# Kernel tuning notes

Measured on AMD Instinct MI355X. Metric: run time of the kernel, lower is better.

Reference implementation:

```python
import jax, jax.numpy as jnp
import numpy as np

N_NODES = 50000


def gcn_conv(x, W, b, src, dst, n_nodes):
    """PyG GCNConv: h = x @ W; symmetric-normalized aggregation with self-loops; + bias."""
    h = x @ W  # [N, F_out]
    ones = jnp.ones(src.shape[0], dtype=h.dtype)
    # degree including the self-loop (edge weight 1)
    deg = jax.ops.segment_sum(ones, dst, num_segments=n_nodes) + 1.0
    dinv = jax.lax.rsqrt(deg)  # deg >= 1, always valid
    norm = dinv[src] * dinv[dst]  # [E]
    msgs = h[src] * norm[:, None]  # [E, F_out]
    agg = jax.ops.segment_sum(msgs, dst, num_segments=n_nodes)
    agg = agg + h * (dinv * dinv)[:, None]  # self-loop contribution, norm = dinv_i^2
    return agg + b


def setup_inputs() -> dict:
    key = jax.random.key(0)
    ks = jax.random.split(key, 8)
    n, f_in, f_hid, f_out, n_edges = N_NODES, 128, 128, 40, 800000
    x = jax.random.normal(ks[0], (n, f_in), dtype=jnp.float32)
    edge_index = jax.random.randint(ks[1], (2, n_edges), 0, n, dtype=jnp.int64)
    new_edge_indexs = jax.random.randint(ks[2], (2, 1000), 0, n, dtype=jnp.int64)
    # Glorot init like PyG defaults
    s1 = (6.0 / (f_in + f_hid)) ** 0.5
    s2 = (6.0 / (f_hid + f_out)) ** 0.5
    W1 = jax.random.uniform(ks[3], (f_in, f_hid), jnp.float32, -s1, s1)
    b1 = jnp.zeros((f_hid,), jnp.float32)
    W2 = jax.random.uniform(ks[4], (f_hid, f_out), jnp.float32, -s2, s2)
    b2 = jnp.zeros((f_out,), jnp.float32)
    return {"x": x, "W1": W1, "b1": b1, "W2": W2, "b2": b2,
            "edge_index": edge_index, "new_edge_indexs": new_edge_indexs}


def reference(x, W1, b1, W2, b2, edge_index, new_edge_indexs):
    src, dst = edge_index[0], edge_index[1]
    h = gcn_conv(x, W1, b1, src, dst, N_NODES)
    h = jax.nn.relu(h)
    # dropout(p=0.5) is identity in eval mode (training=False)
    h = gcn_conv(h, W2, b2, src, dst, N_NODES)
    return jax.nn.log_softmax(h, axis=-1)
```

## Files before the change

kernel.cpp:

```cpp
#include <hip/hip_runtime.h>
#include <hip/hip_bf16.h>

#define N_NODES 50000
#define N_EDGES 800000
#define F_IN    128
#define F_HID   128
#define F_OUT   40
#define F_OUT_P 64
#define N_TILES (N_NODES / 16)

#define NBIN      98
#define BIN_SHIFT 9
#define EPB       1024
#define CAP       32
#define GBIN_CAP  9216

#define CVT_BLOCKS ((F_IN * F_HID + F_OUT_P * F_HID) / 256)
#define BIN_BLOCKS ((N_EDGES + EPB - 1) / EPB)
#define G1_BLOCKS  ((N_TILES + 3) / 4)

typedef __attribute__((ext_vector_type(8))) short bf16x8;
typedef __attribute__((ext_vector_type(4))) float f32x4;

__device__ __forceinline__ float2 unpack_bf2(unsigned u) {
    float2 r;
    r.x = __uint_as_float(u << 16);
    r.y = __uint_as_float(u & 0xffff0000u);
    return r;
}
__device__ __forceinline__ unsigned pack_bf2(float x, float y) {
    union { unsigned u; __hip_bfloat16 h[2]; } cv;
    cv.h[0] = __float2bfloat16(x);
    cv.h[1] = __float2bfloat16(y);
    return cv.u;
}
__device__ __forceinline__ short bfraw(float v) {
    __hip_bfloat16 h = __float2bfloat16(v);
    return *(short*)&h;
}
__device__ __forceinline__ float bf16u_to_f32(unsigned short us) {
    return __uint_as_float(((unsigned)us) << 16);
}
__device__ __forceinline__ unsigned f32_to_h16(float v) {
    _Float16 h = (_Float16)v;
    return (unsigned)*(unsigned short*)&h;
}
__device__ __forceinline__ float h16_to_f32(unsigned bits) {
    unsigned short us = (unsigned short)bits;
    _Float16 h = *(_Float16*)&us;
    return (float)h;
}

__device__ __forceinline__ int ld_src(const unsigned int* w, int is64, int e) {
    return is64 ? (int)w[2 * e] : (int)w[e];
}
__device__ __forceinline__ int ld_dst(const unsigned int* w, int is64, int e) {
    return is64 ? (int)w[2 * (N_EDGES + e)] : (int)w[N_EDGES + e];
}

__global__ void k_init(const unsigned int* __restrict__ ew,
                       const float* __restrict__ W1, const float* __restrict__ W2,
                       __hip_bfloat16* __restrict__ w1t, __hip_bfloat16* __restrict__ w2t,
                       int* __restrict__ flag, int* __restrict__ gcnt) {
    int b = blockIdx.x, t = threadIdx.x;
    if (b < CVT_BLOCKS) {
        int idx = b * 256 + t;
        if (idx < F_IN * F_HID) {
            int n = idx >> 7, k = idx & 127;
            w1t[idx] = __float2bfloat16(W1[k * F_HID + n]);
        } else {
            int j = idx - F_IN * F_HID;
            int n = j >> 7, k = j & 127;
            w2t[j] = __float2bfloat16(n < F_OUT ? W2[k * F_OUT + n] : 0.f);
        }
        return;
    }
    __shared__ int nz;
    if (t == 0) nz = 0;
    __syncthreads();
    int local = 0;
    for (int i = t; i < 4096; i += 256)
        if (ew[2 * i + 1] != 0u) local = 1;
    if (local) atomicOr(&nz, 1);
    if (t < NBIN) gcnt[t] = 0;
    __syncthreads();
    if (t == 0) flag[0] = (nz == 0) ? 1 : 0;
}

__global__ void k_bing1(const unsigned int* __restrict__ ew, const int* __restrict__ flag,
                        int* __restrict__ gcnt, unsigned* __restrict__ gbin,
                        const float* __restrict__ x, const __hip_bfloat16* __restrict__ w1t,
                        __hip_bfloat16* __restrict__ h1b) {
    __shared__ unsigned buf[NBIN][CAP];
    __shared__ int cnt[NBIN];
    __shared__ int base[NBIN];
    int t = threadIdx.x;
    if (blockIdx.x < BIN_BLOCKS) {
        for (int i = t; i < NBIN; i += 256) cnt[i] = 0;
        __syncthreads();
        int is64 = flag[0];
        int e0 = blockIdx.x * EPB;
        int n = min(EPB, N_EDGES - e0);
        if (n == EPB) {
            int s[4], d[4];
#pragma unroll
            for (int j = 0; j < 4; j++) {
                int e = e0 + t + j * 256;
                s[j] = ld_src(ew, is64, e);
                d[j] = ld_dst(ew, is64, e);
            }
#pragma unroll
            for (int j = 0; j < 4; j++) {
                unsigned rec = (unsigned)s[j] | ((unsigned)d[j] << 16);
                int b = d[j] >> BIN_SHIFT;
                int c = atomicAdd(&cnt[b], 1);
                if (c < CAP) buf[b][c] = rec;
                else {
                    int g = atomicAdd(&gcnt[b], 1);
                    gbin[(size_t)b * GBIN_CAP + g] = rec;
                }
            }
        } else {
            for (int i = t; i < n; i += 256) {
                int e = e0 + i;
                int s = ld_src(ew, is64, e), d = ld_dst(ew, is64, e);
                unsigned rec = (unsigned)s | ((unsigned)d << 16);
                int b = d >> BIN_SHIFT;
                int c = atomicAdd(&cnt[b], 1);
                if (c < CAP) buf[b][c] = rec;
                else {
                    int g = atomicAdd(&gcnt[b], 1);
                    gbin[(size_t)b * GBIN_CAP + g] = rec;
                }
            }
        }
        __syncthreads();
        if (t < NBIN) {
            int m = min(cnt[t], CAP);
            base[t] = atomicAdd(&gcnt[t], m);
            cnt[t] = m;
        }
        __syncthreads();
        int wave = t >> 6, lane = t & 63;
        for (int b = wave; b < NBIN; b += 4) {
            int m = cnt[b], bs = base[b];
            for (int i = lane; i < m; i += 64)
                gbin[(size_t)b * GBIN_CAP + bs + i] = buf[b][i];
        }
        return;
    }
    int wave = t >> 6, lane = t & 63;
    int tile = (blockIdx.x - BIN_BLOCKS) * 4 + wave;
    if (tile >= N_TILES) return;
    int node0 = tile * 16;
    int m = lane & 15, q = lane >> 4;
    bf16x8 A[4];
    const float* arow = x + (size_t)(node0 + m) * F_IN + q * 8;
#pragma unroll
    for (int kt = 0; kt < 4; kt++) {
        float4 f0 = *(const float4*)(arow + kt * 32);
        float4 f1 = *(const float4*)(arow + kt * 32 + 4);
        bf16x8 a;
        a[0] = bfraw(f0.x); a[1] = bfraw(f0.y); a[2] = bfraw(f0.z); a[3] = bfraw(f0.w);
        a[4] = bfraw(f1.x); a[5] = bfraw(f1.y); a[6] = bfraw(f1.z); a[7] = bfraw(f1.w);
        A[kt] = a;
    }
#pragma unroll
    for (int c = 0; c < 8; c++) {
        f32x4 acc = {0.f, 0.f, 0.f, 0.f};
        const __hip_bfloat16* brow = w1t + (size_t)(c * 16 + m) * F_IN + q * 8;
#pragma unroll
        for (int kt = 0; kt < 4; kt++) {
            bf16x8 B = *(const bf16x8*)(brow + kt * 32);
            acc = __builtin_amdgcn_mfma_f32_16x16x32_bf16(A[kt], B, acc, 0, 0, 0);
        }
#pragma unroll
        for (int r = 0; r < 4; r++)
            h1b[(size_t)(node0 + q * 4 + r) * F_HID + c * 16 + m] = __float2bfloat16(acc[r]);
    }
}

__global__ void k_passB1(const int* __restrict__ gcnt, const unsigned* __restrict__ gbin,
                         int* __restrict__ rowptr, float* __restrict__ dinv) {
    __shared__ int c[512];
    __shared__ int s2[256];
    __shared__ int gall[NBIN];
    __shared__ int bbase;
    int t = threadIdx.x;
    int b = blockIdx.x;
    c[t] = 0; c[t + 256] = 0;
    if (t < NBIN) gall[t] = gcnt[t];
    __syncthreads();
    if (t == 0) {
        int s = 0;
        for (int i = 0; i < b; i++) s += gall[i];
        bbase = s;
    }
    int n = gall[b];
    const unsigned* rec = gbin + (size_t)b * GBIN_CAP;
    int base512 = b << BIN_SHIFT;
    for (int i = t; i < n; i += 256)
        atomicAdd(&c[(int)(rec[i] >> 16) - base512], 1);
    __syncthreads();
    int a0 = c[2 * t], a1 = c[2 * t + 1];
    s2[t] = a0 + a1;
    __syncthreads();
    for (int off = 1; off < 256; off <<= 1) {
        int u = (t >= off) ? s2[t - off] : 0;
        __syncthreads();
        s2[t] += u;
        __syncthreads();
    }
    int ebase = bbase + s2[t] - a0 - a1;
    int i0 = base512 + 2 * t, i1 = i0 + 1;
    if (i0 < N_NODES) { rowptr[i0] = ebase;      dinv[i0] = rsqrtf((float)a0 + 1.f); }
    if (i1 < N_NODES) { rowptr[i1] = ebase + a0; dinv[i1] = rsqrtf((float)a1 + 1.f); }
    if (b == 0 && t == 0) rowptr[N_NODES] = N_EDGES;
}

__global__ void k_passB2(const int* __restrict__ gcnt, const unsigned* __restrict__ gbin,
                         const int* __restrict__ rowptr, const float* __restrict__ dinv,
                         unsigned* __restrict__ srcw) {
    __shared__ int pos[512];
    __shared__ float dloc[512];
    int t = threadIdx.x;
    int b = blockIdx.x;
    int base512 = b << BIN_SHIFT;
#pragma unroll
    for (int k = 0; k < 2; k++) {
        int j = t + k * 256;
        int i = base512 + j;
        pos[j]  = (i < N_NODES) ? rowptr[i] : 0;
        dloc[j] = (i < N_NODES) ? dinv[i] : 0.f;
    }
    __syncthreads();
    int n = gcnt[b];
    const unsigned* rec = gbin + (size_t)b * GBIN_CAP;
    for (int i = t; i < n; i += 256) {
        unsigned r = rec[i];
        int s  = (int)(r & 0xFFFFu);
        int dl = (int)(r >> 16) - base512;
        int slot = atomicAdd(&pos[dl], 1);
        float norm = dinv[s] * dloc[dl];
        srcw[slot] = (unsigned)s | (f32_to_h16(norm) << 16);
    }
}

__global__ void k_agg1g2(const int* __restrict__ rowptr, const unsigned* __restrict__ srcw,
                         const float* __restrict__ dinv, const __hip_bfloat16* __restrict__ h1b,
                         const float* __restrict__ b1, const __hip_bfloat16* __restrict__ w2t,
                         __hip_bfloat16* __restrict__ h2b) {
    __shared__ __align__(16) short h1r[16][136];
    int t = threadIdx.x, wave = t >> 6, lane = t & 63;
    int node0 = blockIdx.x * 16;
    const unsigned* h1u = (const unsigned*)h1b;
#pragma unroll
    for (int i = 0; i < 4; i++) {
        int row = wave * 4 + i;
        int node = node0 + row;
        float di = dinv[node];
        int beg = __builtin_amdgcn_readfirstlane(rowptr[node]);
        int end = __builtin_amdgcn_readfirstlane(rowptr[node + 1]);
        float2 acc = unpack_bf2(h1u[(size_t)node * 64 + lane]);
        float w0 = di * di;
        acc.x *= w0; acc.y *= w0;
        int e = beg;
        for (; e + 7 < end; e += 8) {
            unsigned p[8];
#pragma unroll
            for (int j = 0; j < 8; j++) p[j] = srcw[e + j];
            unsigned u[8];
#pragma unroll
            for (int j = 0; j < 8; j++)
                u[j] = h1u[(size_t)(p[j] & 0xFFFFu) * 64 + lane];
#pragma unroll
            for (int j = 0; j < 8; j++) {
                float w = h16_to_f32(p[j] >> 16);
                float2 v = unpack_bf2(u[j]);
                acc.x += v.x * w;
                acc.y += v.y * w;
            }
        }
        for (; e < end; e++) {
            unsigned p = srcw[e];
            float w = h16_to_f32(p >> 16);
            float2 v = unpack_bf2(h1u[(size_t)(p & 0xFFFFu) * 64 + lane]);
            acc.x += v.x * w;
            acc.y += v.y * w;
        }
        float2 bb = ((const float2*)b1)[lane];
        acc.x = fmaxf(acc.x + bb.x, 0.f);
        acc.y = fmaxf(acc.y + bb.y, 0.f);
        ((unsigned*)&h1r[row][0])[lane] = pack_bf2(acc.x, acc.y);
    }
    __syncthreads();
    {
        int m = lane & 15, q = lane >> 4;
        bf16x8 A[4];
#pragma unroll
        for (int kt = 0; kt < 4; kt++)
            A[kt] = *(const bf16x8*)(&h1r[m][q * 8 + kt * 32]);
        int c = wave;
        f32x4 acc = {0.f, 0.f, 0.f, 0.f};
        const __hip_bfloat16* brow = w2t + (size_t)(c * 16 + m) * F_HID + q * 8;
#pragma unroll
        for (int kt = 0; kt < 4; kt++) {
            bf16x8 B = *(const bf16x8*)(brow + kt * 32);
            acc = __builtin_amdgcn_mfma_f32_16x16x32_bf16(A[kt], B, acc, 0, 0, 0);
        }
        int col = c * 16 + m;
#pragma unroll
        for (int r = 0; r < 4; r++)
            h2b[(size_t)(node0 + q * 4 + r) * F_OUT_P + col] = __float2bfloat16(acc[r]);
    }
}

__global__ void k_agg2f(const int* __restrict__ rowptr, const unsigned* __restrict__ srcw,
                        const float* __restrict__ dinv,
                        const unsigned short* __restrict__ h2b,
                        const float* __restrict__ b2, float* __restrict__ out) {
    int wave = threadIdx.x >> 6, lane = threadIdx.x & 63;
    int node = blockIdx.x * 4 + wave;
    float di = dinv[node];
    int beg = __builtin_amdgcn_readfirstlane(rowptr[node]);
    int end = __builtin_amdgcn_readfirstlane(rowptr[node + 1]);
    float acc = bf16u_to_f32(h2b[(size_t)node * F_OUT_P + lane]) * di * di;
    int e = beg;
    for (; e + 7 < end; e += 8) {
        unsigned p[8];
#pragma unroll
        for (int j = 0; j < 8; j++) p[j] = srcw[e + j];
        float v[8];
#pragma unroll
        for (int j = 0; j < 8; j++)
            v[j] = bf16u_to_f32(h2b[(size_t)(p[j] & 0xFFFFu) * F_OUT_P + lane]);
#pragma unroll
        for (int j = 0; j < 8; j++)
            acc += v[j] * h16_to_f32(p[j] >> 16);
    }
    for (; e < end; e++) {
        unsigned p = srcw[e];
        acc += bf16u_to_f32(h2b[(size_t)(p & 0xFFFFu) * F_OUT_P + lane]) * h16_to_f32(p >> 16);
    }
    float v = (lane < F_OUT) ? acc + b2[lane] : -INFINITY;
    float m = v;
    for (int off = 32; off; off >>= 1) m = fmaxf(m, __shfl_xor(m, off));
    float ex = (lane < F_OUT) ? __expf(v - m) : 0.f;
    float ssum = ex;
    for (int off = 32; off; off >>= 1) ssum += __shfl_xor(ssum, off);
    float ls = __logf(ssum);
    if (lane < F_OUT)
        out[(size_t)node * F_OUT + lane] = v - m - ls;
}

extern "C" void kernel_launch(void* const* d_in, const int* in_sizes, int n_in,
                              void* d_out, int out_size, void* d_ws, size_t ws_size,
                              hipStream_t stream) {
    const float* x  = (const float*)d_in[0];
    const float* W1 = (const float*)d_in[1];
    const float* b1 = (const float*)d_in[2];
    const float* W2 = (const float*)d_in[3];
    const float* b2 = (const float*)d_in[4];
    const unsigned int* ew = (const unsigned int*)d_in[5];
    float* out = (float*)d_out;

    char* ws = (char*)d_ws;
    int*   flag     = (int*)ws;   ws += 256;
    int*   gcnt     = (int*)ws;   ws += 512;
    float* dinv     = (float*)ws; ws += ((N_NODES * 4 + 255) / 256) * 256;
    int*   rowptr   = (int*)ws;   ws += (((N_NODES + 1) * 4 + 255) / 256) * 256;
    unsigned* gbin  = (unsigned*)ws; ws += (size_t)NBIN * GBIN_CAP * 4;
    unsigned* srcw  = (unsigned*)ws; ws += (size_t)N_EDGES * 4;
    __hip_bfloat16* w1t  = (__hip_bfloat16*)ws; ws += F_IN * F_HID * 2;
    __hip_bfloat16* w2t  = (__hip_bfloat16*)ws; ws += F_OUT_P * F_HID * 2;
    __hip_bfloat16* h1b  = (__hip_bfloat16*)ws; ws += (size_t)N_NODES * F_HID * 2;
    __hip_bfloat16* h2b  = (__hip_bfloat16*)ws; ws += (size_t)N_NODES * F_OUT_P * 2;

    k_init   <<<CVT_BLOCKS + 1, 256, 0, stream>>>(ew, W1, W2, w1t, w2t, flag, gcnt);
    k_bing1  <<<BIN_BLOCKS + G1_BLOCKS, 256, 0, stream>>>(ew, flag, gcnt, gbin, x, w1t, h1b);
    k_passB1 <<<NBIN, 256, 0, stream>>>(gcnt, gbin, rowptr, dinv);
    k_passB2 <<<NBIN, 256, 0, stream>>>(gcnt, gbin, rowptr, dinv, srcw);
    k_agg1g2 <<<N_NODES / 16, 256, 0, stream>>>(rowptr, srcw, dinv, h1b, b1, w2t, h2b);
    k_agg2f  <<<N_NODES / 4, 256, 0, stream>>>(rowptr, srcw, dinv,
                                               (const unsigned short*)h2b, b2, out);
}
```

Measured before the change: 207.6 us.

## Merge CSR passes into one kernel and compute edge norms on the fly

Fuses the two CSR-building passes into a single kernel that keeps scatter positions in shared memory, removing one launch and the global rowptr/dinv reloads. The per-edge fp16 normalization weight is no longer precomputed and packed into srcw. The aggregation kernels instead gather dinv[src] per edge and multiply by the destination's dinv. This trades a cheaper build phase for an extra random 4-byte gather per edge in both aggregation passes, though it also avoids the fp16 rounding of the weights.

```diff
diff --git a/kernel.cpp b/kernel.cpp
--- a/kernel.cpp
+++ b/kernel.cpp
@@ -40,15 +40,6 @@
 }
 __device__ __forceinline__ float bf16u_to_f32(unsigned short us) {
     return __uint_as_float(((unsigned)us) << 16);
-}
-__device__ __forceinline__ unsigned f32_to_h16(float v) {
-    _Float16 h = (_Float16)v;
-    return (unsigned)*(unsigned short*)&h;
-}
-__device__ __forceinline__ float h16_to_f32(unsigned bits) {
-    unsigned short us = (unsigned short)bits;
-    _Float16 h = *(_Float16*)&us;
-    return (float)h;
 }
 
 __device__ __forceinline__ int ld_src(const unsigned int* w, int is64, int e) {
@@ -180,12 +171,14 @@
     }
 }
 
-__global__ void k_passB1(const int* __restrict__ gcnt, const unsigned* __restrict__ gbin,
-                         int* __restrict__ rowptr, float* __restrict__ dinv) {
+__global__ void k_passB(const int* __restrict__ gcnt, const unsigned* __restrict__ gbin,
+                        int* __restrict__ rowptr, float* __restrict__ dinv,
+                        unsigned* __restrict__ srcw) {
     __shared__ int c[512];
     __shared__ int s2[256];
     __shared__ int gall[NBIN];
     __shared__ int bbase;
+    __shared__ int pos[512];
     int t = threadIdx.x;
     int b = blockIdx.x;
     c[t] = 0; c[t + 256] = 0;
@@ -215,34 +208,15 @@
     int i0 = base512 + 2 * t, i1 = i0 + 1;
     if (i0 < N_NODES) { rowptr[i0] = ebase;      dinv[i0] = rsqrtf((float)a0 + 1.f); }
     if (i1 < N_NODES) { rowptr[i1] = ebase + a0; dinv[i1] = rsqrtf((float)a1 + 1.f); }
+    pos[2 * t]     = ebase;
+    pos[2 * t + 1] = ebase + a0;
     if (b == 0 && t == 0) rowptr[N_NODES] = N_EDGES;
-}
-
-__global__ void k_passB2(const int* __restrict__ gcnt, const unsigned* __restrict__ gbin,
-                         const int* __restrict__ rowptr, const float* __restrict__ dinv,
-                         unsigned* __restrict__ srcw) {
-    __shared__ int pos[512];
-    __shared__ float dloc[512];
-    int t = threadIdx.x;
-    int b = blockIdx.x;
-    int base512 = b << BIN_SHIFT;
-#pragma unroll
-    for (int k = 0; k < 2; k++) {
-        int j = t + k * 256;
-        int i = base512 + j;
-        pos[j]  = (i < N_NODES) ? rowptr[i] : 0;
-        dloc[j] = (i < N_NODES) ? dinv[i] : 0.f;
-    }
-    __syncthreads();
-    int n = gcnt[b];
-    const unsigned* rec = gbin + (size_t)b * GBIN_CAP;
+    __syncthreads();
     for (int i = t; i < n; i += 256) {
         unsigned r = rec[i];
-        int s  = (int)(r & 0xFFFFu);
         int dl = (int)(r >> 16) - base512;
         int slot = atomicAdd(&pos[dl], 1);
-        float norm = dinv[s] * dloc[dl];
-        srcw[slot] = (unsigned)s | (f32_to_h16(norm) << 16);
+        srcw[slot] = r & 0xFFFFu;
     }
 }
 
@@ -269,13 +243,16 @@
             unsigned p[8];
 #pragma unroll
             for (int j = 0; j < 8; j++) p[j] = srcw[e + j];
+            float ws[8];
+#pragma unroll
+            for (int j = 0; j < 8; j++) ws[j] = dinv[p[j]];
             unsigned u[8];
 #pragma unroll
             for (int j = 0; j < 8; j++)
-                u[j] = h1u[(size_t)(p[j] & 0xFFFFu) * 64 + lane];
+                u[j] = h1u[(size_t)p[j] * 64 + lane];
 #pragma unroll
             for (int j = 0; j < 8; j++) {
-                float w = h16_to_f32(p[j] >> 16);
+                float w = ws[j] * di;
                 float2 v = unpack_bf2(u[j]);
                 acc.x += v.x * w;
                 acc.y += v.y * w;
@@ -283,8 +260,8 @@
         }
         for (; e < end; e++) {
             unsigned p = srcw[e];
-            float w = h16_to_f32(p >> 16);
-            float2 v = unpack_bf2(h1u[(size_t)(p & 0xFFFFu) * 64 + lane]);
+            float w = dinv[p] * di;
+            float2 v = unpack_bf2(h1u[(size_t)p * 64 + lane]);
             acc.x += v.x * w;
             acc.y += v.y * w;
         }
@@ -330,17 +307,20 @@
         unsigned p[8];
 #pragma unroll
         for (int j = 0; j < 8; j++) p[j] = srcw[e + j];
+        float ws[8];
+#pragma unroll
+        for (int j = 0; j < 8; j++) ws[j] = dinv[p[j]];
         float v[8];
 #pragma unroll
         for (int j = 0; j < 8; j++)
-            v[j] = bf16u_to_f32(h2b[(size_t)(p[j] & 0xFFFFu) * F_OUT_P + lane]);
+            v[j] = bf16u_to_f32(h2b[(size_t)p[j] * F_OUT_P + lane]);
 #pragma unroll
         for (int j = 0; j < 8; j++)
-            acc += v[j] * h16_to_f32(p[j] >> 16);
+            acc += v[j] * (ws[j] * di);
     }
     for (; e < end; e++) {
         unsigned p = srcw[e];
-        acc += bf16u_to_f32(h2b[(size_t)(p & 0xFFFFu) * F_OUT_P + lane]) * h16_to_f32(p >> 16);
+        acc += bf16u_to_f32(h2b[(size_t)p * F_OUT_P + lane]) * (dinv[p] * di);
     }
     float v = (lane < F_OUT) ? acc + b2[lane] : -INFINITY;
     float m = v;
@@ -378,8 +358,7 @@
 
     k_init   <<<CVT_BLOCKS + 1, 256, 0, stream>>>(ew, W1, W2, w1t, w2t, flag, gcnt);
     k_bing1  <<<BIN_BLOCKS + G1_BLOCKS, 256, 0, stream>>>(ew, flag, gcnt, gbin, x, w1t, h1b);
-    k_passB1 <<<NBIN, 256, 0, stream>>>(gcnt, gbin, rowptr, dinv);
-    k_passB2 <<<NBIN, 256, 0, stream>>>(gcnt, gbin, rowptr, dinv, srcw);
+    k_passB  <<<NBIN, 256, 0, stream>>>(gcnt, gbin, rowptr, dinv, srcw);
     k_agg1g2 <<<N_NODES / 16, 256, 0, stream>>>(rowptr, srcw, dinv, h1b, b1, w2t, h2b);
     k_agg2f  <<<N_NODES / 4, 256, 0, stream>>>(rowptr, srcw, dinv,
                                                (const unsigned short*)h2b, b2, out);
```

After: 210.1 us. No clear change (+1.2%).
